# Kernel optimization log

Hardware: AMD Instinct MI355X
Metric: run time of the kernel (lower is better)

Reference implementation:

```python
import jax, jax.numpy as jnp
import numpy as np

B, C, H, W = 16, 3, 320, 448
N_ITERS = 5
LAMBDA = 0.01          # geom_weight
HUBER_DELTA = 0.1      # robust m-estimator threshold
EPS = 1e-6


def skew3(w):
    # [..., 3] -> [..., 3, 3]
    x, y, z = w[..., 0], w[..., 1], w[..., 2]
    O = jnp.zeros_like(x)
    return jnp.stack([jnp.stack([O, -z, y], -1),
                      jnp.stack([z, O, -x], -1),
                      jnp.stack([-y, x, O], -1)], -2)


def se3_exp(xi):
    # xi = [v, w] [B,6] -> T [B,4,4]
    v, w = xi[:, :3], xi[:, 3:]
    th2 = jnp.sum(w * w, -1)[:, None, None]
    th2c = jnp.maximum(th2, 1e-16)
    th = jnp.sqrt(th2c)
    small = th2 < 1e-10
    A = jnp.where(small, 1.0 - th2 / 6.0, jnp.sin(th) / th)
    Bc = jnp.where(small, 0.5 - th2 / 24.0, (1.0 - jnp.cos(th)) / th2c)
    Cc = jnp.where(small, 1.0 / 6.0 - th2 / 120.0, (1.0 - A) / th2c)
    K = skew3(w)
    K2 = K @ K
    I = jnp.eye(3, dtype=xi.dtype)
    R = I + A * K + Bc * K2
    V = I + Bc * K + Cc * K2
    t = jnp.einsum('bij,bj->bi', V, v)
    T = jnp.zeros((xi.shape[0], 4, 4), xi.dtype)
    return T.at[:, :3, :3].set(R).at[:, :3, 3].set(t).at[:, 3, 3].set(1.0)


def feature_gradient(img):
    # central differences with replicated edges, [B,C,H,W] -> (dx, dy) same shape
    p = jnp.pad(img, ((0, 0), (0, 0), (0, 0), (1, 1)), mode='edge')
    dx = 0.5 * (p[..., 2:] - p[..., :-2])
    p = jnp.pad(img, ((0, 0), (0, 0), (1, 1), (0, 0)), mode='edge')
    dy = 0.5 * (p[..., 2:, :] - p[..., :-2, :])
    return dx, dy


def grid_sample(img, grid):
    # bilinear, zeros padding, align_corners=True. img [B,C,H,W], grid [B,H,W,2] in [-1,1]
    Bi, Ci, Hi, Wi = img.shape
    ix = (grid[..., 0] + 1.0) * 0.5 * (Wi - 1)
    iy = (grid[..., 1] + 1.0) * 0.5 * (Hi - 1)
    x0 = jnp.floor(ix)
    y0 = jnp.floor(iy)
    wx1 = ix - x0
    wy1 = iy - y0
    flat = img.reshape(Bi, Ci, Hi * Wi)
    def gather(xf, yf):
        inb = (xf >= 0) & (xf <= Wi - 1) & (yf >= 0) & (yf <= Hi - 1)
        xc = jnp.clip(xf.astype(jnp.int32), 0, Wi - 1)
        yc = jnp.clip(yf.astype(jnp.int32), 0, Hi - 1)
        lin = (yc * Wi + xc).reshape(Bi, 1, -1)
        vals = jnp.take_along_axis(flat, lin, axis=2).reshape(Bi, Ci, xf.shape[1], xf.shape[2])
        return vals * inb[:, None].astype(img.dtype)
    return (gather(x0, y0) * ((1 - wx1) * (1 - wy1))[:, None]
            + gather(x0 + 1, y0) * (wx1 * (1 - wy1))[:, None]
            + gather(x0, y0 + 1) * ((1 - wx1) * wy1)[:, None]
            + gather(x0 + 1, y0 + 1) * (wx1 * wy1)[:, None])


def projective_transform(T, invD1, intr, jacobian):
    # warp pixels of frame 1 into frame 0 using pose T and inverse depth invD1
    fx, fy, cx, cy = [intr[:, i][:, None, None] for i in range(4)]
    dt = invD1.dtype
    uu = jnp.arange(W, dtype=dt)[None, None, :]
    vv = jnp.arange(H, dtype=dt)[None, :, None]
    iD = jnp.maximum(invD1[:, 0], EPS)             # [B,H,W]
    z1 = 1.0 / iD
    x1 = (uu - cx) / fx * z1
    y1 = (vv - cy) / fy * z1
    X1 = jnp.stack([x1, y1, z1], -1)               # [B,H,W,3]
    R, t = T[:, :3, :3], T[:, :3, 3]
    X0 = jnp.einsum('bij,bhwj->bhwi', R, X1) + t[:, None, None, :]
    z0 = X0[..., 2]
    z0s = jnp.where(jnp.abs(z0) > EPS, z0, EPS)
    iz = 1.0 / z0s
    u0 = fx * X0[..., 0] * iz + cx
    v0 = fy * X0[..., 1] * iz + cy
    x0 = jnp.stack([u0, v0, iz], 1)                # [B,3,H,W] (u, v, inverse depth)
    valid = (z0 > EPS) & (invD1[:, 0] > EPS)       # [B,H,W]
    if not jacobian:
        return x0, valid
    O = jnp.zeros_like(z0)
    # Jp = d(u0,v0)/dX0 [B,H,W,2,3]
    Jp = jnp.stack([jnp.stack([fx * iz, O, -fx * X0[..., 0] * iz * iz], -1),
                    jnp.stack([O, fy * iz, -fy * X0[..., 1] * iz * iz], -1)], -2)
    # Jt = dX0/dxi = [I3 | -skew(X0)] [B,H,W,3,6]
    I3 = jnp.broadcast_to(jnp.eye(3, dtype=dt), (X0.shape[0], H, W, 3, 3))
    Jt = jnp.concatenate([I3, -skew3(X0)], -1)
    return x0, valid, Jp, Jt


def align(pose_twist, I0, I1, invD0, invD1, intrinsics):
    T = se3_exp(pose_twist)
    # pre-computable inverse-compositional Jacobian pieces (at initial pose)
    _, _, Jp, Jt = projective_transform(T, invD1, intrinsics, True)
    Jw = jnp.einsum('bhwij,bhwjk->bhwik', Jp, Jt)  # [B,H,W,2,6]
    Jt_z = Jt[..., 2, :]                           # [B,H,W,6]
    dI0_dx, dI0_dy = feature_gradient(I0)
    dD0_dx, dD0_dy = feature_gradient(invD0)
    Bsz = I0.shape[0]
    for _ in range(N_ITERS):
        x0, valid = projective_transform(T, invD1, intrinsics, False)
        u_, v_, d_ = x0[:, 0], x0[:, 1], x0[:, 2]
        inb = (u_ > 0) & (u_ < W - 1) & (v_ > 0) & (v_ < H - 1)
        vmask = (inb & valid)[:, None]             # [B,1,H,W]
        grid = jnp.clip((jnp.stack([u_ / (W - 1), v_ / (H - 1)], -1) - 0.5) * 2.0, -2.0, 2.0)
        grad_I0 = jnp.stack([grid_sample(dI0_dx, grid), grid_sample(dI0_dy, grid)], -1)  # [B,C,H,W,2]
        grad_D0 = jnp.stack([grid_sample(dD0_dx, grid), grid_sample(dD0_dy, grid)], -1)  # [B,1,H,W,2]
        r_I = jnp.where(vmask, I1 - grid_sample(I0, grid), 1e-6)
        r_Z = jnp.where(vmask, d_[:, None] - grid_sample(invD0, grid), 1e-6)
        J_I = -jnp.einsum('bchwn,bhwnx->bchwx', grad_I0, Jw)
        J_Z = -(jnp.einsum('bchwn,bhwnx->bchwx', grad_D0, Jw) - Jt_z[:, None])
        J = jnp.concatenate([J_I.reshape(Bsz, -1, 6), LAMBDA * J_Z.reshape(Bsz, -1, 6)], 1)
        r = jnp.concatenate([r_I.reshape(Bsz, -1), LAMBDA * r_Z.reshape(Bsz, -1)], 1)
        # Huber robust weights
        wts = jnp.minimum(1.0, HUBER_DELTA / jnp.maximum(jnp.abs(r), EPS))
        JtWJ = jnp.einsum('bnx,bny->bxy', J, wts[..., None] * J)     # [B,6,6]
        tr = jnp.trace(JtWJ, axis1=-2, axis2=-1)
        Hm = JtWJ + (tr * 1e-6)[:, None, None] * jnp.eye(6, dtype=J.dtype)  # LM damping
        Rhs = jnp.einsum('bnx,bn->bx', J, wts * r)
        xi = jnp.linalg.solve(Hm, Rhs[..., None])[..., 0]
        # pose = pose * exp(xi)^{-1} = pose @ exp(-xi)
        T = T @ se3_exp(-xi)
    return T


def setup_inputs():
    key = jax.random.key(0)
    ks = jax.random.split(key, 6)
    pose_twist = 0.01 * jax.random.normal(ks[0], (B, 6), jnp.float32)
    I0 = jax.random.uniform(ks[1], (B, C, H, W), dtype=jnp.float32)
    I1 = jax.random.uniform(ks[2], (B, C, H, W), dtype=jnp.float32)
    invD0 = 0.2 + 0.8 * jax.random.uniform(ks[3], (B, 1, H, W), dtype=jnp.float32)
    invD1 = 0.2 + 0.8 * jax.random.uniform(ks[4], (B, 1, H, W), dtype=jnp.float32)
    intr = jnp.tile(jnp.array([[1.1 * W, 1.1 * W, (W - 1) / 2.0, (H - 1) / 2.0]], jnp.float32), (B, 1))
    return {"pose_twist": pose_twist, "I0": I0, "I1": I1,
            "invD0": invD0, "invD1": invD1, "intrinsics": intr}


def reference(pose_twist, I0, I1, invD0, invD1, intrinsics):
    return align(pose_twist, I0, I1, invD0, invD1, intrinsics)
```

## Files before the change

### kernel.cpp

```cpp
#include <hip/hip_runtime.h>
#include <hip/hip_fp16.h>
#include <math.h>

#define B_ 16
#define C_ 3
#define H_ 320
#define W_ 448
#define HW_ (H_*W_)
#define NITERS_ 5
#define LAMBDA_ 0.01f
#define HUBER_ 0.1f
#define EPS_ 1e-6f

#define BPB 112
#define CHUNK 1280
#define TPB 256
#define PPT 5

#define PARTIALS_OFF 2048
#define PLANE_OFF    262144
#define PLANE_U4     ((size_t)B_*HW_)
#define WS_NEED      (PLANE_OFF + PLANE_U4*16)

typedef __attribute__((__vector_size__(2 * sizeof(float)))) float vfloat2;

__device__ __host__ inline void se3_exp_d(const double xi[6], double T[16]) {
    double vx = xi[0], vy = xi[1], vz = xi[2];
    double wx = xi[3], wy = xi[4], wz = xi[5];
    double th2  = wx*wx + wy*wy + wz*wz;
    double th2c = th2 > 1e-16 ? th2 : 1e-16;
    double th   = sqrt(th2c);
    bool   sm   = th2 < 1e-10;
    double A  = sm ? (1.0 - th2*(1.0/6.0))   : (sin(th)/th);
    double Bc = sm ? (0.5 - th2*(1.0/24.0))  : ((1.0 - cos(th))/th2c);
    double Cc = sm ? (1.0/6.0 - th2*(1.0/120.0)) : ((1.0 - A)/th2c);
    double K[9]  = {0.0,-wz,wy,  wz,0.0,-wx,  -wy,wx,0.0};
    double K2[9];
    #pragma unroll
    for (int i = 0; i < 3; ++i)
        #pragma unroll
        for (int j = 0; j < 3; ++j) {
            double s = 0.0;
            #pragma unroll
            for (int k = 0; k < 3; ++k) s += K[i*3+k]*K[k*3+j];
            K2[i*3+j] = s;
        }
    double R[9], V[9];
    #pragma unroll
    for (int i = 0; i < 9; ++i) {
        double I = (i == 0 || i == 4 || i == 8) ? 1.0 : 0.0;
        R[i] = I + A*K[i]  + Bc*K2[i];
        V[i] = I + Bc*K[i] + Cc*K2[i];
    }
    double tx = V[0]*vx + V[1]*vy + V[2]*vz;
    double ty = V[3]*vx + V[4]*vy + V[5]*vz;
    double tz = V[6]*vx + V[7]*vy + V[8]*vz;
    T[0]=R[0]; T[1]=R[1]; T[2] =R[2]; T[3] =tx;
    T[4]=R[3]; T[5]=R[4]; T[6] =R[5]; T[7] =ty;
    T[8]=R[6]; T[9]=R[7]; T[10]=R[8]; T[11]=tz;
    T[12]=0.0; T[13]=0.0; T[14]=0.0;  T[15]=1.0;
}

__global__ void init_kernel(const float* __restrict__ pose,
                            float* __restrict__ Tcur, float* __restrict__ Tinit) {
    int b = threadIdx.x;
    if (b >= B_) return;
    double xi[6];
    #pragma unroll
    for (int k = 0; k < 6; ++k) xi[k] = (double)pose[b*6+k];
    double T[16];
    se3_exp_d(xi, T);
    #pragma unroll
    for (int k = 0; k < 16; ++k) {
        float f = (float)T[k];
        Tcur[b*16+k]  = f;
        Tinit[b*16+k] = f;
    }
}

#define PRE_BPB (HW_/TPB)
__device__ __forceinline__ unsigned pk16(float a, float b) {
    __half2 h = __floats2half2_rn(a, b);
    unsigned u; __builtin_memcpy(&u, &h, 4); return u;
}
__global__ __launch_bounds__(TPB)
void pack_kernel(const float* __restrict__ I0, const float* __restrict__ invD0,
                 uint4* __restrict__ P4)
{
    const int b   = blockIdx.x / PRE_BPB;
    const int rem = blockIdx.x % PRE_BPB;
    const int p   = rem*TPB + (int)threadIdx.x;
    const int y   = p / W_;
    const int x   = p - y*W_;
    const int xp  = (x < W_-1) ? 1 : 0;
    const int xm  = (x > 0) ? -1 : 0;
    const int yp  = (y < H_-1) ? W_ : 0;
    const int ym  = (y > 0) ? -W_ : 0;

    const float* s0 = I0    + (size_t)b*C_*HW_ + p;
    const float* sd = invD0 + (size_t)b*HW_   + p;

    const float v0 = s0[0], v1 = s0[HW_], v2 = s0[2*HW_], v3 = sd[0];
    const float dx0 = 0.5f*(s0[xp]       - s0[xm]);
    const float dx1 = 0.5f*(s0[HW_+xp]   - s0[HW_+xm]);
    const float dx2 = 0.5f*(s0[2*HW_+xp] - s0[2*HW_+xm]);
    const float dx3 = 0.5f*(sd[xp]       - sd[xm]);
    const float dy0 = 0.5f*(s0[yp]       - s0[ym]);
    const float dy1 = 0.5f*(s0[HW_+yp]   - s0[HW_+ym]);
    const float dy2 = 0.5f*(s0[2*HW_+yp] - s0[2*HW_+ym]);
    const float dy3 = 0.5f*(sd[yp]       - sd[ym]);

    int zx = 0, zy = 0;
    zx = __builtin_amdgcn_cvt_pk_fp8_f32(dx0, dx1, zx, false);
    zx = __builtin_amdgcn_cvt_pk_fp8_f32(dx2, dx3, zx, true);
    zy = __builtin_amdgcn_cvt_pk_fp8_f32(dy0, dy1, zy, false);
    zy = __builtin_amdgcn_cvt_pk_fp8_f32(dy2, dy3, zy, true);

    P4[(size_t)b*HW_ + p] = make_uint4(pk16(v0,v1), pk16(v2,v3),
                                       (unsigned)zx, (unsigned)zy);
}

__device__ __forceinline__ __half2 bc2(unsigned u) {
    __half2 h; __builtin_memcpy(&h, &u, 4); return h;
}
__device__ __forceinline__ float2 h2f(__half2 h) { return __half22float2(h); }

__global__ __launch_bounds__(TPB)
void pixel_h8_kernel(const uint4* __restrict__ P4,
                     const float* __restrict__ I1, const float* __restrict__ invD1,
                     const float* __restrict__ intr,
                     const float* __restrict__ Tcur, const float* __restrict__ Tinit,
                     float* __restrict__ partials)
{
    const int nwg = B_*BPB;
    const int bid = blockIdx.x;
    const int swz = (bid & 7) * (nwg >> 3) + (bid >> 3);
    const int b   = swz / BPB;
    const int blk = swz % BPB;

    const float fx = intr[b*4+0], fy = intr[b*4+1];
    const float cx = intr[b*4+2], cy = intr[b*4+3];
    const float inv_fx = 1.0f/fx, inv_fy = 1.0f/fy;

    const float* Tc = Tcur  + b*16;
    const float* Ti = Tinit + b*16;
    const float Rc00=Tc[0], Rc01=Tc[1], Rc02=Tc[2],  tcx=Tc[3];
    const float Rc10=Tc[4], Rc11=Tc[5], Rc12=Tc[6],  tcy=Tc[7];
    const float Rc20=Tc[8], Rc21=Tc[9], Rc22=Tc[10], tcz=Tc[11];
    const float Ri00=Ti[0], Ri01=Ti[1], Ri02=Ti[2],  tix=Ti[3];
    const float Ri10=Ti[4], Ri11=Ti[5], Ri12=Ti[6],  tiy=Ti[7];
    const float Ri20=Ti[8], Ri21=Ti[9], Ri22=Ti[10], tiz=Ti[11];

    const uint4* Pb = P4 + (size_t)b*HW_;
    const float* P1 = I1    + (size_t)b*C_*HW_;
    const float* D1 = invD1 + (size_t)b*HW_;

    float acc[27];
    #pragma unroll
    for (int k = 0; k < 27; ++k) acc[k] = 0.0f;

    const int base = blk*CHUNK + (int)threadIdx.x;

    float d1v[PPT];
    #pragma unroll
    for (int i = 0; i < PPT; ++i) d1v[i] = D1[base + i*TPB];

    auto body = [&](int i5) {
        const int p = base + i5*TPB;
        const int vcoord = p / W_;
        const int ucoord = p - vcoord*W_;

        const float p1a = P1[p];
        const float p1b = P1[HW_ + p];
        const float p1c = P1[2*HW_ + p];

        const float iD1 = d1v[i5];
        const float iD  = fmaxf(iD1, EPS_);
        const float z1  = 1.0f / iD;
        const float x1  = ((float)ucoord - cx)*inv_fx * z1;
        const float y1  = ((float)vcoord - cy)*inv_fy * z1;

        const float Xc0 = Rc00*x1 + Rc01*y1 + Rc02*z1 + tcx;
        const float Xc1 = Rc10*x1 + Rc11*y1 + Rc12*z1 + tcy;
        const float Xc2 = Rc20*x1 + Rc21*y1 + Rc22*z1 + tcz;
        const float z0s = (fabsf(Xc2) > EPS_) ? Xc2 : EPS_;
        const float izc = 1.0f / z0s;
        const float u0  = fx*Xc0*izc + cx;
        const float v0  = fy*Xc1*izc + cy;
        const bool valid = (Xc2 > EPS_) && (iD1 > EPS_);
        const bool inb   = (u0 > 0.0f) && (u0 < (float)(W_-1)) &&
                           (v0 > 0.0f) && (v0 < (float)(H_-1));
        const bool vm = valid && inb;

        const float Xi0 = Ri00*x1 + Ri01*y1 + Ri02*z1 + tix;
        const float Xi1 = Ri10*x1 + Ri11*y1 + Ri12*z1 + tiy;
        const float Xi2 = Ri20*x1 + Ri21*y1 + Ri22*z1 + tiz;
        const float zis = (fabsf(Xi2) > EPS_) ? Xi2 : EPS_;
        const float izi = 1.0f / zis;
        const float aJ = fx*izi;
        const float cJ = -fx*Xi0*izi*izi;
        const float bJ = fy*izi;
        const float dJ = -fy*Xi1*izi*izi;

        const float gx = fminf(fmaxf((u0/(float)(W_-1) - 0.5f)*2.0f, -2.0f), 2.0f);
        const float gy = fminf(fmaxf((v0/(float)(H_-1) - 0.5f)*2.0f, -2.0f), 2.0f);
        const float ix = (gx + 1.0f)*0.5f*(float)(W_-1);
        const float iy = (gy + 1.0f)*0.5f*(float)(H_-1);
        const float x0f = floorf(ix), y0f = floorf(iy);
        const float wx1 = ix - x0f,  wy1 = iy - y0f;
        const float wx0 = 1.0f - wx1, wy0 = 1.0f - wy1;

        const bool bx0 = (x0f >= 0.0f)  && (x0f <= (float)(W_-1));
        const bool bx1 = (x0f >= -1.0f) && (x0f <= (float)(W_-2));
        const bool by0 = (y0f >= 0.0f)  && (y0f <= (float)(H_-1));
        const bool by1 = (y0f >= -1.0f) && (y0f <= (float)(H_-2));
        const float m00 = (bx0 && by0) ? wx0*wy0 : 0.0f;
        const float m10 = (bx1 && by0) ? wx1*wy0 : 0.0f;
        const float m01 = (bx0 && by1) ? wx0*wy1 : 0.0f;
        const float m11 = (bx1 && by1) ? wx1*wy1 : 0.0f;

        const int x0i = (int)x0f;
        const int y0i = (int)y0f;
        const int c0 = min(max(x0i,   0), W_-1);
        const int c1 = min(max(x0i+1, 0), W_-1);
        const int o0 = min(max(y0i,   0), H_-1) * W_;
        const int o1 = min(max(y0i+1, 0), H_-1) * W_;

        const uint4 A00 = Pb[o0+c0];
        const uint4 A10 = Pb[o0+c1];
        const uint4 A01 = Pb[o1+c0];
        const uint4 A11 = Pb[o1+c1];

        float sv0=0,sv1=0,sv2=0,sv3=0;
        float gx0=0,gx1=0,gx2=0,gx3=0;
        float gy0=0,gy1=0,gy2=0,gy3=0;
        #define BLEND(A, m) {                                               \
            float2 t;                                                       \
            t = h2f(bc2(A.x)); sv0 += m*t.x; sv1 += m*t.y;                  \
            t = h2f(bc2(A.y)); sv2 += m*t.x; sv3 += m*t.y;                  \
            vfloat2 g0 = __builtin_amdgcn_cvt_pk_f32_fp8((int)A.z, false);  \
            gx0 += m*g0[0]; gx1 += m*g0[1];                                 \
            vfloat2 g1 = __builtin_amdgcn_cvt_pk_f32_fp8((int)A.z, true);   \
            gx2 += m*g1[0]; gx3 += m*g1[1];                                 \
            vfloat2 g2 = __builtin_amdgcn_cvt_pk_f32_fp8((int)A.w, false);  \
            gy0 += m*g2[0]; gy1 += m*g2[1];                                 \
            vfloat2 g3 = __builtin_amdgcn_cvt_pk_f32_fp8((int)A.w, true);   \
            gy2 += m*g3[0]; gy3 += m*g3[1]; }
        BLEND(A00, m00)
        BLEND(A10, m10)
        BLEND(A01, m01)
        BLEND(A11, m11)
        #undef BLEND

        float S00=0,S01=0,S02=0,S11=0,S12=0,S22=0, U0=0,U1=0,U2=0;
        #define PHOTO(SVc, GXc, GYc, P1c) {                            \
            const float r  = vm ? (P1c - SVc) : 1e-6f;                 \
            const float w  = fminf(1.0f, HUBER_ / fmaxf(fabsf(r), EPS_)); \
            const float hx = GXc*aJ, hy = GYc*bJ, hz_ = GXc*cJ + GYc*dJ;  \
            const float whx = w*hx, why = w*hy, wr = w*r;              \
            S00 += whx*hx; S01 += whx*hy; S02 += whx*hz_;              \
            S11 += why*hy; S12 += why*hz_; S22 += w*hz_*hz_;           \
            U0 -= wr*hx; U1 -= wr*hy; U2 -= wr*hz_; }
        PHOTO(sv0, gx0, gy0, p1a)
        PHOTO(sv1, gx1, gy1, p1b)
        PHOTO(sv2, gx2, gy2, p1c)
        #undef PHOTO
        {
            const float rz = LAMBDA_*(vm ? (izc - sv3) : 1e-6f);
            const float w  = fminf(1.0f, HUBER_ / fmaxf(fabsf(rz), EPS_));
            const float hx = gx3*aJ, hy = gy3*bJ, hz_ = gx3*cJ + gy3*dJ;
            const float qx = -hx, qy = -hy, qz = 1.0f - hz_;
            const float wl2 = w*(LAMBDA_*LAMBDA_);
            const float wqx = wl2*qx, wqy = wl2*qy;
            S00 += wqx*qx; S01 += wqx*qy; S02 += wqx*qz;
            S11 += wqy*qy; S12 += wqy*qz; S22 += wl2*qz*qz;
            const float wrl = w*rz*LAMBDA_;
            U0 += wrl*qx; U1 += wrl*qy; U2 += wrl*qz;
        }
        const float x = Xi0, y = Xi1, z = Xi2;
        const float P00 =  S01*z - S02*y, P01 = -S00*z + S02*x, P02 =  S00*y - S01*x;
        const float P10 =  S11*z - S12*y, P11 = -S01*z + S12*x, P12 =  S01*y - S11*x;
        const float P20 =  S12*z - S22*y, P21 = -S02*z + S22*x, P22 =  S02*y - S12*x;
        const float Q00 =  z*P10 - y*P20, Q01 =  z*P11 - y*P21, Q02 =  z*P12 - y*P22;
        const float Q11 = -z*P01 + x*P21, Q12 = -z*P02 + x*P22;
        const float Q22 =  y*P02 - x*P12;
        acc[0]  += S00; acc[1]  += S01; acc[2]  += S02;
        acc[3]  += S11; acc[4]  += S12; acc[5]  += S22;
        acc[6]  -= P00; acc[7]  -= P01; acc[8]  -= P02;
        acc[9]  -= P10; acc[10] -= P11; acc[11] -= P12;
        acc[12] -= P20; acc[13] -= P21; acc[14] -= P22;
        acc[15] += Q00; acc[16] += Q01; acc[17] += Q02;
        acc[18] += Q11; acc[19] += Q12; acc[20] += Q22;
        acc[21] += U0; acc[22] += U1; acc[23] += U2;
        acc[24] += y*U2 - z*U1;
        acc[25] += z*U0 - x*U2;
        acc[26] += x*U1 - y*U0;
    };

    #pragma unroll
    for (int i5 = 0; i5 < PPT; ++i5)
        body(i5);

    #pragma unroll
    for (int off = 32; off >= 1; off >>= 1) {
        #pragma unroll
        for (int k = 0; k < 27; ++k)
            acc[k] += __shfl_down(acc[k], off);
    }
    __shared__ float red[TPB/64][27];
    const int lane = threadIdx.x & 63;
    const int wid  = threadIdx.x >> 6;
    if (lane == 0) {
        #pragma unroll
        for (int k = 0; k < 27; ++k) red[wid][k] = acc[k];
    }
    __syncthreads();
    if (threadIdx.x < 27) {
        float s = red[0][threadIdx.x] + red[1][threadIdx.x]
                + red[2][threadIdx.x] + red[3][threadIdx.x];
        partials[((size_t)b*BPB + blk)*27 + threadIdx.x] = s;
    }
}

__global__ void solve_kernel(const float* __restrict__ partials,
                             float* __restrict__ Tcur, float* __restrict__ out)
{
    const int b = blockIdx.x;
    __shared__ double S[27];
    const int t = threadIdx.x;
    if (t < 27) {
        double s = 0.0;
        const float* pp = partials + (size_t)b*BPB*27 + t;
        for (int blk = 0; blk < BPB; ++blk) s += (double)pp[blk*27];
        S[t] = s;
    }
    __syncthreads();
    if (t == 0) {
        double Hm[6][6], rhs[6];
        Hm[0][0]=S[0];  Hm[0][1]=S[1];  Hm[0][2]=S[2];
        Hm[1][1]=S[3];  Hm[1][2]=S[4];  Hm[2][2]=S[5];
        for (int i = 0; i < 3; ++i)
            for (int j = 0; j < 3; ++j)
                Hm[i][3+j] = S[6 + i*3 + j];
        Hm[3][3]=S[15]; Hm[3][4]=S[16]; Hm[3][5]=S[17];
        Hm[4][4]=S[18]; Hm[4][5]=S[19]; Hm[5][5]=S[20];
        for (int i = 0; i < 6; ++i)
            for (int j = 0; j < i; ++j) Hm[i][j] = Hm[j][i];
        for (int i = 0; i < 6; ++i) rhs[i] = S[21+i];

        double tr = 0.0;
        for (int i = 0; i < 6; ++i) tr += Hm[i][i];
        const double damp = tr*1e-6;
        for (int i = 0; i < 6; ++i) Hm[i][i] += damp;

        double M[6][7];
        for (int i = 0; i < 6; ++i) {
            for (int j = 0; j < 6; ++j) M[i][j] = Hm[i][j];
            M[i][6] = rhs[i];
        }
        for (int col = 0; col < 6; ++col) {
            int piv = col; double mx = fabs(M[col][col]);
            for (int r2 = col+1; r2 < 6; ++r2) {
                double a2 = fabs(M[r2][col]);
                if (a2 > mx) { mx = a2; piv = r2; }
            }
            if (piv != col)
                for (int j = col; j < 7; ++j) {
                    double tmp = M[col][j]; M[col][j] = M[piv][j]; M[piv][j] = tmp;
                }
            const double inv = 1.0 / M[col][col];
            for (int r2 = col+1; r2 < 6; ++r2) {
                const double f = M[r2][col]*inv;
                for (int j = col; j < 7; ++j) M[r2][j] -= f*M[col][j];
            }
        }
        double xi[6];
        for (int i = 5; i >= 0; --i) {
            double s2 = M[i][6];
            for (int j = i+1; j < 6; ++j) s2 -= M[i][j]*xi[j];
            xi[i] = s2 / M[i][i];
        }
        double nxi[6];
        for (int i = 0; i < 6; ++i) nxi[i] = -xi[i];
        double E[16];
        se3_exp_d(nxi, E);

        double Tc[16];
        for (int k = 0; k < 16; ++k) Tc[k] = (double)Tcur[b*16+k];
        for (int i = 0; i < 4; ++i)
            for (int j = 0; j < 4; ++j) {
                double s2 = 0.0;
                for (int k = 0; k < 4; ++k) s2 += Tc[i*4+k]*E[k*4+j];
                const float f = (float)s2;
                Tcur[b*16 + i*4 + j] = f;
                out[b*16 + i*4 + j]  = f;
            }
    }
}

extern "C" void kernel_launch(void* const* d_in, const int* in_sizes, int n_in,
                              void* d_out, int out_size, void* d_ws, size_t ws_size,
                              hipStream_t stream) {
    const float* pose  = (const float*)d_in[0];
    const float* I0    = (const float*)d_in[1];
    const float* I1    = (const float*)d_in[2];
    const float* invD0 = (const float*)d_in[3];
    const float* invD1 = (const float*)d_in[4];
    const float* intr  = (const float*)d_in[5];
    float* out = (float*)d_out;

    float* Tcur     = (float*)d_ws;
    float* Tinit    = Tcur + 256;
    float* partials = (float*)((char*)d_ws + PARTIALS_OFF);
    uint4* P4       = (uint4*)((char*)d_ws + PLANE_OFF);

    hipLaunchKernelGGL(init_kernel, dim3(1), dim3(64), 0, stream, pose, Tcur, Tinit);
    hipLaunchKernelGGL(pack_kernel, dim3(B_*PRE_BPB), dim3(TPB), 0, stream,
                       I0, invD0, P4);
    for (int it = 0; it < NITERS_; ++it) {
        hipLaunchKernelGGL(pixel_h8_kernel, dim3(B_*BPB), dim3(TPB), 0, stream,
                           P4, I1, invD1, intr, Tcur, Tinit, partials);
        hipLaunchKernelGGL(solve_kernel, dim3(B_), dim3(64), 0, stream,
                           partials, Tcur, out);
    }
}
```

Baseline: 274.5 us.

## Precompute initial-pose 3D points and use relative transform per iteration

The pack kernel now computes each pixel's 3D point under the initial pose once and stores it, together with invD1, as a float4 plane. Each iteration maps those points with a delta transform Tcur·Tinit⁻¹ computed in the solve kernel, so the per-pixel unprojection and second rigid transform are no longer redone every iteration. This trades ALU work for an extra 16 bytes per pixel read per iteration (replacing a 4-byte invD1 read) and a larger workspace. Composing through the delta in float may also change numerical rounding slightly.

```diff
diff --git a/kernel.cpp b/kernel.cpp
--- a/kernel.cpp
+++ b/kernel.cpp
@@ -18,9 +18,10 @@
 #define PPT 5
 
 #define PARTIALS_OFF 2048
+#define DMAT_OFF     200704
 #define PLANE_OFF    262144
 #define PLANE_U4     ((size_t)B_*HW_)
-#define WS_NEED      (PLANE_OFF + PLANE_U4*16)
+#define XI_OFF       (PLANE_OFF + PLANE_U4*16)
 
 typedef __attribute__((__vector_size__(2 * sizeof(float)))) float vfloat2;
 
@@ -61,8 +62,31 @@
     T[12]=0.0; T[13]=0.0; T[14]=0.0;  T[15]=1.0;
 }
 
+__device__ inline void write_delta(const double Tc[16], const float* Ti,
+                                   float* Dm) {
+    double Ri[9], ti[3];
+    Ri[0]=Ti[0]; Ri[1]=Ti[1]; Ri[2]=Ti[2];  ti[0]=Ti[3];
+    Ri[3]=Ti[4]; Ri[4]=Ti[5]; Ri[5]=Ti[6];  ti[1]=Ti[7];
+    Ri[6]=Ti[8]; Ri[7]=Ti[9]; Ri[8]=Ti[10]; ti[2]=Ti[11];
+    double D[9];
+    #pragma unroll
+    for (int i = 0; i < 3; ++i)
+        #pragma unroll
+        for (int j = 0; j < 3; ++j)
+            D[i*3+j] = Tc[i*4+0]*Ri[j*3+0] + Tc[i*4+1]*Ri[j*3+1] + Tc[i*4+2]*Ri[j*3+2];
+    #pragma unroll
+    for (int i = 0; i < 3; ++i) {
+        const double di = Tc[i*4+3] - (D[i*3+0]*ti[0] + D[i*3+1]*ti[1] + D[i*3+2]*ti[2]);
+        Dm[i*4+0] = (float)D[i*3+0];
+        Dm[i*4+1] = (float)D[i*3+1];
+        Dm[i*4+2] = (float)D[i*3+2];
+        Dm[i*4+3] = (float)di;
+    }
+}
+
 __global__ void init_kernel(const float* __restrict__ pose,
-                            float* __restrict__ Tcur, float* __restrict__ Tinit) {
+                            float* __restrict__ Tcur, float* __restrict__ Tinit,
+                            float* __restrict__ Dmat) {
     int b = threadIdx.x;
     if (b >= B_) return;
     double xi[6];
@@ -76,6 +100,7 @@
         Tcur[b*16+k]  = f;
         Tinit[b*16+k] = f;
     }
+    write_delta(T, Tinit + b*16, Dmat + b*12);
 }
 
 #define PRE_BPB (HW_/TPB)
@@ -85,7 +110,9 @@
 }
 __global__ __launch_bounds__(TPB)
 void pack_kernel(const float* __restrict__ I0, const float* __restrict__ invD0,
-                 uint4* __restrict__ P4)
+                 const float* __restrict__ invD1, const float* __restrict__ intr,
+                 const float* __restrict__ Tinit,
+                 uint4* __restrict__ P4, float4* __restrict__ XI4)
 {
     const int b   = blockIdx.x / PRE_BPB;
     const int rem = blockIdx.x % PRE_BPB;
@@ -118,6 +145,19 @@
 
     P4[(size_t)b*HW_ + p] = make_uint4(pk16(v0,v1), pk16(v2,v3),
                                        (unsigned)zx, (unsigned)zy);
+
+    const float fx = intr[b*4+0], fy = intr[b*4+1];
+    const float cx = intr[b*4+2], cy = intr[b*4+3];
+    const float* Ti = Tinit + b*16;
+    const float iD1 = invD1[(size_t)b*HW_ + p];
+    const float iD  = fmaxf(iD1, EPS_);
+    const float z1  = 1.0f / iD;
+    const float x1  = ((float)x - cx)/fx * z1;
+    const float y1  = ((float)y - cy)/fy * z1;
+    const float Xi0 = Ti[0]*x1 + Ti[1]*y1 + Ti[2]*z1  + Ti[3];
+    const float Xi1 = Ti[4]*x1 + Ti[5]*y1 + Ti[6]*z1  + Ti[7];
+    const float Xi2 = Ti[8]*x1 + Ti[9]*y1 + Ti[10]*z1 + Ti[11];
+    XI4[(size_t)b*HW_ + p] = make_float4(Xi0, Xi1, Xi2, iD1);
 }
 
 __device__ __forceinline__ __half2 bc2(unsigned u) {
@@ -126,10 +166,10 @@
 __device__ __forceinline__ float2 h2f(__half2 h) { return __half22float2(h); }
 
 __global__ __launch_bounds__(TPB)
-void pixel_h8_kernel(const uint4* __restrict__ P4,
-                     const float* __restrict__ I1, const float* __restrict__ invD1,
+void pixel_xi_kernel(const uint4* __restrict__ P4, const float4* __restrict__ XI4,
+                     const float* __restrict__ I1,
                      const float* __restrict__ intr,
-                     const float* __restrict__ Tcur, const float* __restrict__ Tinit,
+                     const float* __restrict__ Dmat,
                      float* __restrict__ partials)
 {
     const int nwg = B_*BPB;
@@ -140,20 +180,15 @@
 
     const float fx = intr[b*4+0], fy = intr[b*4+1];
     const float cx = intr[b*4+2], cy = intr[b*4+3];
-    const float inv_fx = 1.0f/fx, inv_fy = 1.0f/fy;
-
-    const float* Tc = Tcur  + b*16;
-    const float* Ti = Tinit + b*16;
-    const float Rc00=Tc[0], Rc01=Tc[1], Rc02=Tc[2],  tcx=Tc[3];
-    const float Rc10=Tc[4], Rc11=Tc[5], Rc12=Tc[6],  tcy=Tc[7];
-    const float Rc20=Tc[8], Rc21=Tc[9], Rc22=Tc[10], tcz=Tc[11];
-    const float Ri00=Ti[0], Ri01=Ti[1], Ri02=Ti[2],  tix=Ti[3];
-    const float Ri10=Ti[4], Ri11=Ti[5], Ri12=Ti[6],  tiy=Ti[7];
-    const float Ri20=Ti[8], Ri21=Ti[9], Ri22=Ti[10], tiz=Ti[11];
-
-    const uint4* Pb = P4 + (size_t)b*HW_;
-    const float* P1 = I1    + (size_t)b*C_*HW_;
-    const float* D1 = invD1 + (size_t)b*HW_;
+
+    const float* Dm = Dmat + b*12;
+    const float D00=Dm[0], D01=Dm[1], D02=Dm[2],  d0=Dm[3];
+    const float D10=Dm[4], D11=Dm[5], D12=Dm[6],  d1=Dm[7];
+    const float D20=Dm[8], D21=Dm[9], D22=Dm[10], d2=Dm[11];
+
+    const uint4*  Pb = P4  + (size_t)b*HW_;
+    const float4* Xb = XI4 + (size_t)b*HW_;
+    const float*  P1 = I1  + (size_t)b*C_*HW_;
 
     float acc[27];
     #pragma unroll
@@ -161,28 +196,23 @@
 
     const int base = blk*CHUNK + (int)threadIdx.x;
 
-    float d1v[PPT];
-    #pragma unroll
-    for (int i = 0; i < PPT; ++i) d1v[i] = D1[base + i*TPB];
+    float4 Xiv[PPT];
+    #pragma unroll
+    for (int i = 0; i < PPT; ++i) Xiv[i] = Xb[base + i*TPB];
 
     auto body = [&](int i5) {
         const int p = base + i5*TPB;
-        const int vcoord = p / W_;
-        const int ucoord = p - vcoord*W_;
 
         const float p1a = P1[p];
         const float p1b = P1[HW_ + p];
         const float p1c = P1[2*HW_ + p];
 
-        const float iD1 = d1v[i5];
-        const float iD  = fmaxf(iD1, EPS_);
-        const float z1  = 1.0f / iD;
-        const float x1  = ((float)ucoord - cx)*inv_fx * z1;
-        const float y1  = ((float)vcoord - cy)*inv_fy * z1;
-
-        const float Xc0 = Rc00*x1 + Rc01*y1 + Rc02*z1 + tcx;
-        const float Xc1 = Rc10*x1 + Rc11*y1 + Rc12*z1 + tcy;
-        const float Xc2 = Rc20*x1 + Rc21*y1 + Rc22*z1 + tcz;
+        const float4 F = Xiv[i5];
+        const float iD1 = F.w;
+
+        const float Xc0 = D00*F.x + D01*F.y + D02*F.z + d0;
+        const float Xc1 = D10*F.x + D11*F.y + D12*F.z + d1;
+        const float Xc2 = D20*F.x + D21*F.y + D22*F.z + d2;
         const float z0s = (fabsf(Xc2) > EPS_) ? Xc2 : EPS_;
         const float izc = 1.0f / z0s;
         const float u0  = fx*Xc0*izc + cx;
@@ -192,15 +222,12 @@
                            (v0 > 0.0f) && (v0 < (float)(H_-1));
         const bool vm = valid && inb;
 
-        const float Xi0 = Ri00*x1 + Ri01*y1 + Ri02*z1 + tix;
-        const float Xi1 = Ri10*x1 + Ri11*y1 + Ri12*z1 + tiy;
-        const float Xi2 = Ri20*x1 + Ri21*y1 + Ri22*z1 + tiz;
-        const float zis = (fabsf(Xi2) > EPS_) ? Xi2 : EPS_;
+        const float zis = (fabsf(F.z) > EPS_) ? F.z : EPS_;
         const float izi = 1.0f / zis;
         const float aJ = fx*izi;
-        const float cJ = -fx*Xi0*izi*izi;
+        const float cJ = -fx*F.x*izi*izi;
         const float bJ = fy*izi;
-        const float dJ = -fy*Xi1*izi*izi;
+        const float dJ = -fy*F.y*izi*izi;
 
         const float gx = fminf(fmaxf((u0/(float)(W_-1) - 0.5f)*2.0f, -2.0f), 2.0f);
         const float gy = fminf(fmaxf((v0/(float)(H_-1) - 0.5f)*2.0f, -2.0f), 2.0f);
@@ -277,7 +304,7 @@
             const float wrl = w*rz*LAMBDA_;
             U0 += wrl*qx; U1 += wrl*qy; U2 += wrl*qz;
         }
-        const float x = Xi0, y = Xi1, z = Xi2;
+        const float x = F.x, y = F.y, z = F.z;
         const float P00 =  S01*z - S02*y, P01 = -S00*z + S02*x, P02 =  S00*y - S01*x;
         const float P10 =  S11*z - S12*y, P11 = -S01*z + S12*x, P12 =  S01*y - S11*x;
         const float P20 =  S12*z - S22*y, P21 = -S02*z + S22*x, P22 =  S02*y - S12*x;
@@ -323,7 +350,9 @@
 }
 
 __global__ void solve_kernel(const float* __restrict__ partials,
-                             float* __restrict__ Tcur, float* __restrict__ out)
+                             const float* __restrict__ Tinit,
+                             float* __restrict__ Tcur, float* __restrict__ Dmat,
+                             float* __restrict__ out)
 {
     const int b = blockIdx.x;
     __shared__ double S[27];
@@ -385,16 +414,18 @@
         double E[16];
         se3_exp_d(nxi, E);
 
-        double Tc[16];
+        double Tc[16], Tn[16];
         for (int k = 0; k < 16; ++k) Tc[k] = (double)Tcur[b*16+k];
         for (int i = 0; i < 4; ++i)
             for (int j = 0; j < 4; ++j) {
                 double s2 = 0.0;
                 for (int k = 0; k < 4; ++k) s2 += Tc[i*4+k]*E[k*4+j];
+                Tn[i*4+j] = s2;
                 const float f = (float)s2;
                 Tcur[b*16 + i*4 + j] = f;
                 out[b*16 + i*4 + j]  = f;
             }
+        write_delta(Tn, Tinit + b*16, Dmat + b*12);
     }
 }
 
@@ -409,18 +440,21 @@
     const float* intr  = (const float*)d_in[5];
     float* out = (float*)d_out;
 
-    float* Tcur     = (float*)d_ws;
-    float* Tinit    = Tcur + 256;
-    float* partials = (float*)((char*)d_ws + PARTIALS_OFF);
-    uint4* P4       = (uint4*)((char*)d_ws + PLANE_OFF);
-
-    hipLaunchKernelGGL(init_kernel, dim3(1), dim3(64), 0, stream, pose, Tcur, Tinit);
+    float*  Tcur     = (float*)d_ws;
+    float*  Tinit    = Tcur + 256;
+    float*  partials = (float*)((char*)d_ws + PARTIALS_OFF);
+    float*  Dmat     = (float*)((char*)d_ws + DMAT_OFF);
+    uint4*  P4       = (uint4*)((char*)d_ws + PLANE_OFF);
+    float4* XI4      = (float4*)((char*)d_ws + XI_OFF);
+
+    hipLaunchKernelGGL(init_kernel, dim3(1), dim3(64), 0, stream,
+                       pose, Tcur, Tinit, Dmat);
     hipLaunchKernelGGL(pack_kernel, dim3(B_*PRE_BPB), dim3(TPB), 0, stream,
-                       I0, invD0, P4);
+                       I0, invD0, invD1, intr, Tinit, P4, XI4);
     for (int it = 0; it < NITERS_; ++it) {
-        hipLaunchKernelGGL(pixel_h8_kernel, dim3(B_*BPB), dim3(TPB), 0, stream,
-                           P4, I1, invD1, intr, Tcur, Tinit, partials);
+        hipLaunchKernelGGL(pixel_xi_kernel, dim3(B_*BPB), dim3(TPB), 0, stream,
+                           P4, XI4, I1, intr, Dmat, partials);
         hipLaunchKernelGGL(solve_kernel, dim3(B_), dim3(64), 0, stream,
-                           partials, Tcur, out);
-    }
-}
+                           partials, Tinit, Tcur, Dmat, out);
+    }
+}
```

Result: faster. 268.4 us (-2.2%).
